# Performance work log

Measured on AMD Instinct MI355X. Metric: run time of the kernel, lower is better.

Reference implementation:

```python
import jax, jax.numpy as jnp
import numpy as np

KERNEL_SIZES = [2, 4, 8, 16, 32, 64]
MAXK = max(k + k // 2 for k in KERNEL_SIZES[1:])  # 96
PAD_LO = (MAXK - 1) // 2  # 47
PAD_HI = MAXK - 1 - PAD_LO  # 48


def _alternating(K, even_negative):
    f = np.ones(K, np.float32)
    idx = np.arange(K)
    mask = (idx % 2 == 0) if even_negative else (idx % 2 == 1)
    f[mask] = -1.0
    return f


def make_weight_bank():
    """Builds all 17 fixed filters, zero-padded and center-aligned into one
    (17, 1, MAXK) bank so a single 'same'-padded conv matches 17 torch convs.
    Alignment: torch pads left=(K-1)//2 for kernel K; embedding each kernel at
    offset (MAXK-1)//2 - (K-1)//2 inside a MAXK kernel padded (PAD_LO, PAD_HI)
    reproduces the identical output."""
    filters = []
    for K in KERNEL_SIZES:              # group 1: -1 at even indices
        filters.append(_alternating(K, True))
    for K in KERNEL_SIZES:              # group 2: -1 at odd indices
        filters.append(_alternating(K, False))
    for K in KERNEL_SIZES[1:]:          # group 3: piecewise quadratic, len K + K//2
        q = K // 4
        left = (np.linspace(0.0, 1.0, q + 1, dtype=np.float32)[1:]) ** 2
        right = left[::-1]
        filters.append(np.concatenate([-left, -right, 2 * left, 2 * right, -left, -right]).astype(np.float32))
    W = np.zeros((len(filters), 1, MAXK), np.float32)
    for i, f in enumerate(filters):
        K = len(f)
        o = (MAXK - 1) // 2 - (K - 1) // 2
        W[i, 0, o:o + K] = f
    return jnp.asarray(W)


def setup_inputs() -> dict:
    key = jax.random.key(0)
    x = jax.random.normal(key, (128, 1, 32768), dtype=jnp.float32)
    W = make_weight_bank()  # (17, 1, 96), fixed non-trainable filters
    return {"x": x, "W": W}


def reference(x, W):
    # x: (B, 1, L); W: (17, 1, MAXK). One cross-correlation conv = bank of 17
    # 'same'-padded conv1d filters; then ReLU.
    y = jax.lax.conv_general_dilated(
        x, W,
        window_strides=(1,),
        padding=[(PAD_LO, PAD_HI)],
        dimension_numbers=("NCH", "OIH", "NCH"),
    )
    return jax.nn.relu(y)  # (B, 17, L)
```

## Files before the change

### kernel.cpp

```cpp
#include <hip/hip_runtime.h>


#define S_LEN    32768
#define NFILT    17
#define TILE     1024
#define NTHREADS 256
#define PITCH    284
#define NCHUNK   139

constexpr int Z1_OFF  = 0;
constexpr int Z2_OFF  = Z1_OFF  + TILE + 4;
constexpr int Z4_OFF  = Z2_OFF  + TILE + 8;
constexpr int Z8_OFF  = Z4_OFF  + TILE + 16;
constexpr int Z16_OFF = Z8_OFF  + TILE + 32;
constexpr int ZTOT    = Z16_OFF + TILE + 64;

template<int Qv>
__device__ __forceinline__ float bw(int i) {
    constexpr float inv = 1.0f / (float)Qv;
    const float t = (i < Qv) ? (float)(i + 1) * inv : (float)(2 * Qv - i) * inv;
    return t * t;
}

template<int Qv>
__device__ __forceinline__ void zcalc(const float* __restrict__ xsl,
                                      float* __restrict__ Zf, int bi) {
    constexpr int OFF  = 49 - 3 * Qv;
    constexpr int A0Q  = OFF >> 2;
    constexpr int SH   = OFF & 3;
    constexpr int SPAN = 2 * Qv;
    constexpr int NW   = (SH + SPAN + 3 + 3) >> 2;
    const float4* __restrict__ xs4 =
        reinterpret_cast<const float4*>(xsl) + bi + A0Q;
    float a0 = 0.f, a1 = 0.f, a2 = 0.f, a3 = 0.f;
#pragma unroll
    for (int wi = 0; wi < NW; ++wi) {
        const float4 xw = xs4[wi];
#pragma unroll
        for (int e = 0; e < 4; ++e) {
            const int u = 4 * wi + e - SH;
            const float xv = (e == 0) ? xw.x : (e == 1) ? xw.y
                           : (e == 2) ? xw.z : xw.w;
            if (u >= 0 && u < SPAN)     a0 = fmaf(bw<Qv>(u),     xv, a0);
            if (u >= 1 && u < SPAN + 1) a1 = fmaf(bw<Qv>(u - 1), xv, a1);
            if (u >= 2 && u < SPAN + 2) a2 = fmaf(bw<Qv>(u - 2), xv, a2);
            if (u >= 3 && u < SPAN + 3) a3 = fmaf(bw<Qv>(u - 3), xv, a3);
        }
    }
    reinterpret_cast<float4*>(Zf)[bi] = make_float4(a0, a1, a2, a3);
}

template<int Qv>
__device__ __forceinline__ float4 bump_out(const float* __restrict__ Zf, int tid) {
    const float4* __restrict__ Z4 = reinterpret_cast<const float4*>(Zf);
    const float4 za = Z4[tid];
    float4 y;
    if constexpr (Qv >= 2) {
        const float4 zb = Z4[tid + (Qv >> 1)];
        const float4 zc = Z4[tid + Qv];
        y.x = fmaf(2.f, zb.x, -(za.x + zc.x));
        y.y = fmaf(2.f, zb.y, -(za.y + zc.y));
        y.z = fmaf(2.f, zb.z, -(za.z + zc.z));
        y.w = fmaf(2.f, zb.w, -(za.w + zc.w));
    } else {
        const float4 zb = Z4[tid + 1];
        y.x = fmaf(2.f, za.z, -(za.x + zb.x));
        y.y = fmaf(2.f, za.w, -(za.y + zb.y));
        y.z = fmaf(2.f, zb.x, -(za.z + zb.z));
        y.w = fmaf(2.f, zb.y, -(za.w + zb.w));
    }
    return y;
}

template<int K>
__device__ __forceinline__ float4 alt_acc(const float* __restrict__ Psp, int tid) {
    constexpr int H = (K - 1) / 2;
    float v[4];
#pragma unroll
    for (int r = 0; r < 4; ++r) {
        const int dn  = 48 - H + r;
        const int dn2 = dn + K;
        const float pa = Psp[(dn  & 3) * PITCH + tid + (dn  >> 2)];
        const float pb = Psp[(dn2 & 3) * PITCH + tid + (dn2 >> 2)];
        const float dd = pb - pa;
        v[r] = ((r + H) & 1) ? dd : -dd;
    }
    return make_float4(v[0], v[1], v[2], v[3]);
}

__global__ __launch_bounds__(NTHREADS, 4)
void conv_bank_kernel(const float* __restrict__ x, float* __restrict__ out) {
    __shared__ __align__(16) float xsl[1136];
    __shared__ float Psp[4 * PITCH];
    __shared__ __align__(16) float Zb[ZTOT];
    __shared__ float wtot[2];

    const int tid = threadIdx.x;
    const int bx  = blockIdx.x;
    const int ts  = bx * TILE;
    const int b   = blockIdx.y;
    const float* __restrict__ xrow = x + (size_t)b * S_LEN;

    if (bx >= 1 && bx <= 30) {
        const float4* __restrict__ g4 =
            reinterpret_cast<const float4*>(xrow) + ((ts - 48) >> 2);
        float4* __restrict__ s4 = reinterpret_cast<float4*>(xsl);
#pragma unroll
        for (int i = tid; i < 284; i += NTHREADS)
            s4[i] = (i < 281) ? g4[i] : make_float4(0.f, 0.f, 0.f, 0.f);
    } else {
        for (int j = tid; j < 1136; j += NTHREADS) {
            const int g = ts - 48 + j;
            xsl[j] = (j < 1124 && (unsigned)g < (unsigned)S_LEN) ? xrow[g] : 0.f;
        }
    }
    __syncthreads();

    float4 xa, xb;
    float csum = 0.f, incl;
    {
        const float4* __restrict__ xs4 = reinterpret_cast<const float4*>(xsl);
        if (tid < NCHUNK) {
            xa = xs4[2 * tid];
            xb = xs4[2 * tid + 1];
            csum = (xa.x - xa.y) + (xa.z - xa.w)
                 + (xb.x - xb.y) + (xb.z - xb.w);
        }
        incl = csum;
#pragma unroll
        for (int off = 1; off < 64; off <<= 1) {
            const float v = __shfl_up(incl, off, 64);
            if ((tid & 63) >= off) incl += v;
        }
        if ((tid & 63) == 63 && tid < 128) wtot[tid >> 6] = incl;
    }
    zcalc<16>(xsl, Zb + Z16_OFF, tid);
    zcalc<8 >(xsl, Zb + Z8_OFF,  tid);
    if (tid >= 192 && tid < 208) zcalc<16>(xsl, Zb + Z16_OFF, 256 + (tid - 192));
    if (tid >= 208 && tid < 216) zcalc<8 >(xsl, Zb + Z8_OFF,  256 + (tid - 208));
    __syncthreads();

    zcalc<4>(xsl, Zb + Z4_OFF, tid);
    zcalc<2>(xsl, Zb + Z2_OFF, tid);
    zcalc<1>(xsl, Zb + Z1_OFF, tid);
    if (tid >= 216 && tid < 220) zcalc<4>(xsl, Zb + Z4_OFF, 256 + (tid - 216));
    if (tid >= 220 && tid < 222) zcalc<2>(xsl, Zb + Z2_OFF, 256 + (tid - 220));
    if (tid == 222)              zcalc<1>(xsl, Zb + Z1_OFF, 256);

    if (tid < NCHUNK) {
        float offs = (tid >= 64) ? wtot[0] : 0.f;
        if (tid >= 128) offs += wtot[1];
        float run = offs + (incl - csum);
        float* __restrict__ Pb = Psp + 2 * tid;
        Pb[0 * PITCH + 0] = run; run += xa.x;
        Pb[1 * PITCH + 0] = run; run -= xa.y;
        Pb[2 * PITCH + 0] = run; run += xa.z;
        Pb[3 * PITCH + 0] = run; run -= xa.w;
        Pb[0 * PITCH + 1] = run; run += xb.x;
        Pb[1 * PITCH + 1] = run; run -= xb.y;
        Pb[2 * PITCH + 1] = run; run += xb.z;
        Pb[3 * PITCH + 1] = run;
    }
    __syncthreads();

    const int t0 = ts + 4 * tid;
    float* __restrict__ obase = out + (size_t)b * (NFILT * S_LEN) + t0;

    auto store_relu = [&](int j, float4 v) {
        float4 s;
        s.x = fmaxf(v.x, 0.f); s.y = fmaxf(v.y, 0.f);
        s.z = fmaxf(v.z, 0.f); s.w = fmaxf(v.w, 0.f);
        *reinterpret_cast<float4*>(obase + (size_t)j * S_LEN) = s;
    };
    auto store_pair = [&](int j, float4 a) {
        store_relu(j, a);
        store_relu(j + 6, make_float4(-a.x, -a.y, -a.z, -a.w));
    };

    store_pair(0, alt_acc<2 >(Psp, tid));
    store_pair(1, alt_acc<4 >(Psp, tid));
    store_pair(2, alt_acc<8 >(Psp, tid));
    store_pair(3, alt_acc<16>(Psp, tid));
    store_pair(4, alt_acc<32>(Psp, tid));
    store_pair(5, alt_acc<64>(Psp, tid));

    store_relu(12, bump_out<1 >(Zb + Z1_OFF,  tid));
    store_relu(13, bump_out<2 >(Zb + Z2_OFF,  tid));
    store_relu(14, bump_out<4 >(Zb + Z4_OFF,  tid));
    store_relu(15, bump_out<8 >(Zb + Z8_OFF,  tid));
    store_relu(16, bump_out<16>(Zb + Z16_OFF, tid));
}

extern "C" void kernel_launch(void* const* d_in, const int* in_sizes, int n_in,
                              void* d_out, int out_size, void* d_ws, size_t ws_size,
                              hipStream_t stream) {
    const float* x = (const float*)d_in[0];
    float* out = (float*)d_out;
    const int nbatch = in_sizes[0] / S_LEN;
    dim3 grid(S_LEN / TILE, nbatch, 1);
    conv_bank_kernel<<<grid, NTHREADS, 0, stream>>>(x, out);
}
```

Before: 302.5 us.

## Compute small filters directly and interleave stores between barrier phases

The Z1/Z2 prefix buffers are dropped in favour of direct convolutions for the two smallest bump filters, and the K=2/4 alternating outputs are computed straight from the input tile. Several output stores are moved ahead of the Z4/prefix-sum phase so global writes overlap the remaining shared-memory work. Stores are switched to nontemporal, the final barrier becomes a raw s_barrier after an lgkmcnt wait, and launch bounds are raised to 6 waves per SIMD. This shrinks shared memory and the amount of work after the last barrier, at the cost of extra FMAs for the direct filters and possible register pressure.

```diff
diff --git a/kernel.cpp b/kernel.cpp
--- a/kernel.cpp
+++ b/kernel.cpp
@@ -8,18 +8,28 @@
 #define PITCH    284
 #define NCHUNK   139
 
-constexpr int Z1_OFF  = 0;
-constexpr int Z2_OFF  = Z1_OFF  + TILE + 4;
-constexpr int Z4_OFF  = Z2_OFF  + TILE + 8;
-constexpr int Z8_OFF  = Z4_OFF  + TILE + 16;
-constexpr int Z16_OFF = Z8_OFF  + TILE + 32;
+constexpr int Z4_OFF  = 0;
+constexpr int Z8_OFF  = Z4_OFF + TILE + 16;
+constexpr int Z16_OFF = Z8_OFF + TILE + 32;
 constexpr int ZTOT    = Z16_OFF + TILE + 64;
+
+typedef float fvec4 __attribute__((ext_vector_type(4)));
 
 template<int Qv>
 __device__ __forceinline__ float bw(int i) {
     constexpr float inv = 1.0f / (float)Qv;
     const float t = (i < Qv) ? (float)(i + 1) * inv : (float)(2 * Qv - i) * inv;
     return t * t;
+}
+
+template<int Qv>
+__device__ __forceinline__ float third_w(int j) {
+    constexpr float inv = 1.0f / (float)Qv;
+    const int seg = j / Qv;
+    const int i = j - seg * Qv;
+    const float t = ((seg & 1) == 0) ? (float)(i + 1) * inv : (float)(Qv - i) * inv;
+    const float v = t * t;
+    return (seg == 2 || seg == 3) ? 2.0f * v : -v;
 }
 
 template<int Qv>
@@ -54,22 +64,56 @@
 __device__ __forceinline__ float4 bump_out(const float* __restrict__ Zf, int tid) {
     const float4* __restrict__ Z4 = reinterpret_cast<const float4*>(Zf);
     const float4 za = Z4[tid];
+    const float4 zb = Z4[tid + (Qv >> 1)];
+    const float4 zc = Z4[tid + Qv];
     float4 y;
-    if constexpr (Qv >= 2) {
-        const float4 zb = Z4[tid + (Qv >> 1)];
-        const float4 zc = Z4[tid + Qv];
-        y.x = fmaf(2.f, zb.x, -(za.x + zc.x));
-        y.y = fmaf(2.f, zb.y, -(za.y + zc.y));
-        y.z = fmaf(2.f, zb.z, -(za.z + zc.z));
-        y.w = fmaf(2.f, zb.w, -(za.w + zc.w));
-    } else {
-        const float4 zb = Z4[tid + 1];
-        y.x = fmaf(2.f, za.z, -(za.x + zb.x));
-        y.y = fmaf(2.f, za.w, -(za.y + zb.y));
-        y.z = fmaf(2.f, zb.x, -(za.z + zb.z));
-        y.w = fmaf(2.f, zb.y, -(za.w + zb.w));
-    }
+    y.x = fmaf(2.f, zb.x, -(za.x + zc.x));
+    y.y = fmaf(2.f, zb.y, -(za.y + zc.y));
+    y.z = fmaf(2.f, zb.z, -(za.z + zc.z));
+    y.w = fmaf(2.f, zb.w, -(za.w + zc.w));
     return y;
+}
+
+template<int Qv>
+__device__ __forceinline__ float4 bump_direct(const float* __restrict__ xsl, int tid) {
+    constexpr int SPAN = 6 * Qv;
+    constexpr int C    = (SPAN - 1) / 2;
+    constexpr int OFF  = 48 - C;
+    constexpr int A0   = OFF >> 2;
+    constexpr int SH   = OFF & 3;
+    constexpr int NW   = (SH + SPAN + 3 + 3) >> 2;
+    const float4* __restrict__ xs4 =
+        reinterpret_cast<const float4*>(xsl) + tid + A0;
+    float a0 = 0.f, a1 = 0.f, a2 = 0.f, a3 = 0.f;
+#pragma unroll
+    for (int wi = 0; wi < NW; ++wi) {
+        const float4 xw = xs4[wi];
+#pragma unroll
+        for (int e = 0; e < 4; ++e) {
+            const int u = 4 * wi + e - SH;
+            const float xv = (e == 0) ? xw.x : (e == 1) ? xw.y
+                           : (e == 2) ? xw.z : xw.w;
+            if (u >= 0 && u < SPAN)     a0 = fmaf(third_w<Qv>(u),     xv, a0);
+            if (u >= 1 && u < SPAN + 1) a1 = fmaf(third_w<Qv>(u - 1), xv, a1);
+            if (u >= 2 && u < SPAN + 2) a2 = fmaf(third_w<Qv>(u - 2), xv, a2);
+            if (u >= 3 && u < SPAN + 3) a3 = fmaf(third_w<Qv>(u - 3), xv, a3);
+        }
+    }
+    return make_float4(a0, a1, a2, a3);
+}
+
+__device__ __forceinline__ void alt24_direct(const float* __restrict__ xsl, int tid,
+                                             float4& o2, float4& o4) {
+    const float4* __restrict__ xs4 =
+        reinterpret_cast<const float4*>(xsl) + tid + 11;
+    const float4 wA = xs4[0], wB = xs4[1], wC = xs4[2];
+    const float s3 = wA.w, s4 = wB.x, s5 = wB.y, s6 = wB.z,
+                s7 = wB.w, s8 = wC.x, s9 = wC.y;
+    o2.x = s5 - s4;  o2.y = s6 - s5;  o2.z = s7 - s6;  o2.w = s8 - s7;
+    o4.x = (s4 - s3) + (s6 - s5);
+    o4.y = (s5 - s4) + (s7 - s6);
+    o4.z = (s6 - s5) + (s8 - s7);
+    o4.w = (s7 - s6) + (s9 - s8);
 }
 
 template<int K>
@@ -88,7 +132,7 @@
     return make_float4(v[0], v[1], v[2], v[3]);
 }
 
-__global__ __launch_bounds__(NTHREADS, 4)
+__global__ __launch_bounds__(NTHREADS, 6)
 void conv_bank_kernel(const float* __restrict__ x, float* __restrict__ out) {
     __shared__ __align__(16) float xsl[1136];
     __shared__ float Psp[4 * PITCH];
@@ -140,12 +184,34 @@
     if (tid >= 208 && tid < 216) zcalc<8 >(xsl, Zb + Z8_OFF,  256 + (tid - 208));
     __syncthreads();
 
+    const int t0 = ts + 4 * tid;
+    float* __restrict__ obase = out + (size_t)b * (NFILT * S_LEN) + t0;
+
+    auto store_relu = [&](int j, float4 v) {
+        fvec4 s;
+        s.x = fmaxf(v.x, 0.f); s.y = fmaxf(v.y, 0.f);
+        s.z = fmaxf(v.z, 0.f); s.w = fmaxf(v.w, 0.f);
+        __builtin_nontemporal_store(
+            s, reinterpret_cast<fvec4*>(obase + (size_t)j * S_LEN));
+    };
+    auto store_pair = [&](int j, float4 a) {
+        store_relu(j, a);
+        store_relu(j + 6, make_float4(-a.x, -a.y, -a.z, -a.w));
+    };
+
+    store_relu(16, bump_out<16>(Zb + Z16_OFF, tid));
+    store_relu(15, bump_out<8 >(Zb + Z8_OFF,  tid));
+    store_relu(12, bump_direct<1>(xsl, tid));
+    store_relu(13, bump_direct<2>(xsl, tid));
+    {
+        float4 a2, a4;
+        alt24_direct(xsl, tid, a2, a4);
+        store_pair(0, a2);
+        store_pair(1, a4);
+    }
+
     zcalc<4>(xsl, Zb + Z4_OFF, tid);
-    zcalc<2>(xsl, Zb + Z2_OFF, tid);
-    zcalc<1>(xsl, Zb + Z1_OFF, tid);
     if (tid >= 216 && tid < 220) zcalc<4>(xsl, Zb + Z4_OFF, 256 + (tid - 216));
-    if (tid >= 220 && tid < 222) zcalc<2>(xsl, Zb + Z2_OFF, 256 + (tid - 220));
-    if (tid == 222)              zcalc<1>(xsl, Zb + Z1_OFF, 256);
 
     if (tid < NCHUNK) {
         float offs = (tid >= 64) ? wtot[0] : 0.f;
@@ -161,34 +227,15 @@
         Pb[2 * PITCH + 1] = run; run += xb.z;
         Pb[3 * PITCH + 1] = run;
     }
-    __syncthreads();
-
-    const int t0 = ts + 4 * tid;
-    float* __restrict__ obase = out + (size_t)b * (NFILT * S_LEN) + t0;
-
-    auto store_relu = [&](int j, float4 v) {
-        float4 s;
-        s.x = fmaxf(v.x, 0.f); s.y = fmaxf(v.y, 0.f);
-        s.z = fmaxf(v.z, 0.f); s.w = fmaxf(v.w, 0.f);
-        *reinterpret_cast<float4*>(obase + (size_t)j * S_LEN) = s;
-    };
-    auto store_pair = [&](int j, float4 a) {
-        store_relu(j, a);
-        store_relu(j + 6, make_float4(-a.x, -a.y, -a.z, -a.w));
-    };
-
-    store_pair(0, alt_acc<2 >(Psp, tid));
-    store_pair(1, alt_acc<4 >(Psp, tid));
+
+    asm volatile("s_waitcnt lgkmcnt(0)" ::: "memory");
+    __builtin_amdgcn_s_barrier();
+
     store_pair(2, alt_acc<8 >(Psp, tid));
     store_pair(3, alt_acc<16>(Psp, tid));
     store_pair(4, alt_acc<32>(Psp, tid));
     store_pair(5, alt_acc<64>(Psp, tid));
-
-    store_relu(12, bump_out<1 >(Zb + Z1_OFF,  tid));
-    store_relu(13, bump_out<2 >(Zb + Z2_OFF,  tid));
-    store_relu(14, bump_out<4 >(Zb + Z4_OFF,  tid));
-    store_relu(15, bump_out<8 >(Zb + Z8_OFF,  tid));
-    store_relu(16, bump_out<16>(Zb + Z16_OFF, tid));
+    store_relu(14, bump_out<4>(Zb + Z4_OFF, tid));
 }
 
 extern "C" void kernel_launch(void* const* d_in, const int* in_sizes, int n_in,
```

New measurement: 297.8 us. About the same (-1.6%).
